# Performance work log

Measured on AMD Instinct MI355X. Metric: run time of the kernel, lower is better.

## Reference

```python
import jax, jax.numpy as jnp
import numpy as np

B, N, C, H, W = 32, 32, 3, 32, 32
HID, OUT = 256, 128


def _conv(x, w, b):
    y = jax.lax.conv_general_dilated(
        x, w, window_strides=(1, 1), padding="SAME",
        dimension_numbers=("NCHW", "OIHW", "NCHW"))
    return y + b[None, :, None, None]


def _sage(h, lw, lb, rw):
    # PyG SAGEConv with mean aggregation on a fully-connected graph (no self-loops):
    # agg_i = (sum_j h_j - h_i) / (N-1); out = agg @ lw.T + lb + h @ rw.T
    n = h.shape[1]
    agg = (jnp.sum(h, axis=1, keepdims=True) - h) / (n - 1)
    return jnp.einsum('bnd,od->bno', agg, lw) + lb + jnp.einsum('bnd,od->bno', h, rw)


def setup_inputs() -> dict:
    key = jax.random.key(0)
    ks = jax.random.split(key, 16)
    def g(k, shape, scale):
        return jax.random.normal(k, shape, dtype=jnp.float32) * scale
    return {
        "x": jax.random.normal(ks[0], (B, N, C, H, W), dtype=jnp.float32),
        "mask": jnp.ones((B, N), dtype=jnp.float32),
        "conv1_w": g(ks[1], (64, C, 3, 3), 0.1),
        "conv1_b": jnp.zeros((64,), jnp.float32),
        "conv2_w": g(ks[2], (128, 64, 3, 3), 0.05),
        "conv2_b": jnp.zeros((128,), jnp.float32),
        "fc_w": g(ks[3], (HID, 128), 0.08),
        "fc_b": jnp.zeros((HID,), jnp.float32),
        "s1_lw": g(ks[4], (HID, HID), 0.06),
        "s1_lb": jnp.zeros((HID,), jnp.float32),
        "s1_rw": g(ks[5], (HID, HID), 0.06),
        "s2_lw": g(ks[6], (OUT, HID), 0.06),
        "s2_lb": jnp.zeros((OUT,), jnp.float32),
        "s2_rw": g(ks[7], (OUT, HID), 0.06),
    }


def reference(x, mask, conv1_w, conv1_b, conv2_w, conv2_b, fc_w, fc_b,
              s1_lw, s1_lb, s1_rw, s2_lw, s2_lb, s2_rw):
    b, n, c, h, w = x.shape
    z = x.reshape(b * n, c, h, w)
    z = jax.nn.relu(_conv(z, conv1_w, conv1_b))
    z = jax.nn.relu(_conv(z, conv2_w, conv2_b))
    z = jnp.mean(z, axis=(2, 3))                      # AdaptiveAvgPool2d((1,1)) + flatten
    z = z @ fc_w.T + fc_b                             # [B*N, HID]
    z = z.reshape(b, n, -1) * mask[:, :, None]
    z = jax.nn.relu(_sage(z, s1_lw, s1_lb, s1_rw))
    z = _sage(z, s2_lw, s2_lb, s2_rw)                 # [B, N, OUT]
    return z
```

## Files before the change

kernel.cpp:

```cpp
#include <hip/hip_runtime.h>
#include <hip/hip_bf16.h>


typedef __attribute__((ext_vector_type(8))) short bfrag;
typedef __attribute__((ext_vector_type(4))) float f32x4;
typedef __attribute__((ext_vector_type(16))) float f32x16;

static __device__ __forceinline__ unsigned short f2bf(float f) {
    union { float f; unsigned u; } v; v.f = f;
    unsigned r = v.u + 0x7fff + ((v.u >> 16) & 1);
    return (unsigned short)(r >> 16);
}

static __device__ __forceinline__ unsigned cvtpk(float lo, float hi) {
    unsigned r;
    asm("v_cvt_pk_bf16_f32 %0, %1, %2" : "=v"(r) : "v"(lo), "v"(hi));
    return r;
}

static __device__ __forceinline__ void gl_lds16(const short* g, short* l) {
    __builtin_amdgcn_global_load_lds(
        (const __attribute__((address_space(1))) unsigned int*)g,
        (__attribute__((address_space(3))) unsigned int*)l, 16, 0, 0);
}

__global__ __launch_bounds__(256) void prep_kernel(
    const float* __restrict__ s1lw, const float* __restrict__ s1rw,
    const float* __restrict__ s2lw, const float* __restrict__ s2rw,
    const float* __restrict__ c2w, const float* __restrict__ c1w,
    const float* __restrict__ c1b, const float* __restrict__ fcw,
    float* __restrict__ l1T, float* __restrict__ w1pT,
    float* __restrict__ l2T, float* __restrict__ w2pT,
    float* __restrict__ fwT,
    short* __restrict__ w2c, short* __restrict__ w1b) {
    int i = blockIdx.x * 256 + threadIdx.x;
    const float inv31 = 1.f / 31.f;
    if (i < 65536) {
        int o = i >> 8, d = i & 255;
        float lw = s1lw[i];
        float rw = s1rw[i];
        l1T[d * 256 + o]  = lw;
        w1pT[d * 256 + o] = rw - lw * inv31;
    }
    if (i < 32768) {
        int o = i >> 8, d = i & 255;
        float lw = s2lw[i];
        float rw = s2rw[i];
        l2T[d * 128 + o]  = lw;
        w2pT[d * 128 + o] = rw - lw * inv31;
        int o2 = i >> 7, c = i & 127;
        fwT[c * 256 + o2] = fcw[i];
    }
    if (i < 73728) {
        int oc = i / 576, rem = i - oc * 576;
        int ic = rem / 9, tap = rem - ic * 9;
        int widx = tap * 8192 + (ic >> 4) * 2048 + ((ic >> 3) & 1) * 1024
                 + oc * 8 + (ic & 7);
        w2c[widx] = (short)f2bf(c2w[i]);
    }
    if (i < 2048) {
        int oc = i >> 5, k = i & 31;
        float v = (k < 27) ? c1w[oc * 27 + k] : (k == 27 ? c1b[oc] : 0.f);
        w1b[i] = (short)f2bf(v);
    }
}

__global__ __launch_bounds__(256, 2) void fused_conv_kernel(
    const float* __restrict__ x, const short* __restrict__ w1b,
    const short* __restrict__ w2c, const float* __restrict__ b2,
    float* __restrict__ pooled4) {
    const int band = blockIdx.x, img = blockIdx.y;
    __shared__ short xt[3 * 12 * 34];
    __shared__ short c1t[10 * 34 * 72];
    __shared__ short bufB[3][4096];
    __shared__ float wsum[4][128];
    const int t = threadIdx.x;
    const int w = t >> 6, lane = t & 63;
    const int ln15 = lane & 15, q8 = (lane >> 4) * 8;
    const int ln31 = lane & 31, hi = lane >> 5;

    const float* xi = x + img * 3072;
    for (int idx = t; idx < 1224; idx += 256) {
        int c = idx / 408, rem = idx % 408, r = rem / 34, col = rem % 34;
        int y = band * 8 - 2 + r, xx = col - 1;
        float v = 0.f;
        if ((unsigned)y < 32u && (unsigned)xx < 32u) v = xi[c * 1024 + y * 32 + xx];
        xt[idx] = (short)f2bf(v);
    }
    {
        f32x4 z = {0.f, 0.f, 0.f, 0.f};
        for (int i = t; i < 180; i += 256) {
            int r = i / 18, rem = i % 18, side = rem / 9, q = rem % 9;
            *(f32x4*)(c1t + (r * 34 + side * 33) * 72 + q * 8) = z;
        }
    }
    bfrag b1f[4];
#pragma unroll
    for (int ot = 0; ot < 4; ++ot)
        b1f[ot] = *(const bfrag*)(w1b + (ot * 16 + ln15) * 32 + q8);

    int xOff[8]; int kMask[8]; int kOvr[8];
#pragma unroll
    for (int j = 0; j < 8; ++j) {
        int k = q8 + j;
        int c = (k * 57) >> 9;
        int rem = k - 9 * c;
        int dy = (rem * 11) >> 5;
        int dx = rem - 3 * dy;
        int cc = c < 3 ? c : 2;
        xOff[j] = cc * 408 + dy * 34 + dx;
        kMask[j] = (c < 3) ? 0xFFFF : 0;
        kOvr[j]  = (c < 3) ? 0 : (k == 27 ? 0x3F80 : 0);
    }
    __syncthreads();

    {
        const short* src = w2c + t * 8;
        short* dst = (short*)bufB + t * 8;
        gl_lds16(src, dst);
        gl_lds16(src + 2048, dst + 2048);
        gl_lds16(src + 4096, dst + 4096);
        gl_lds16(src + 6144, dst + 6144);
    }

#pragma unroll 1
    for (int pt = 0; pt < 5; ++pt) {
        const int tile = w * 5 + pt;
        const int r = tile >> 1, xcb = (tile & 1) << 4;
        const int baseA = r * 34 + xcb + ln15;
        bfrag a1f;
#pragma unroll
        for (int j = 0; j < 8; ++j)
            a1f[j] = (short)((xt[xOff[j] + baseA] & kMask[j]) | kOvr[j]);
        f32x4 acc1[4];
#pragma unroll
        for (int ot = 0; ot < 4; ++ot) {
#pragma unroll
            for (int rg = 0; rg < 4; ++rg) acc1[ot][rg] = 0.f;
            acc1[ot] = __builtin_amdgcn_mfma_f32_16x16x32_bf16(
                b1f[ot], a1f, acc1[ot], 0, 0, 0);
        }
        const int y = band * 8 - 1 + r;
        const bool valid = (unsigned)y < 32u;
        const int waddr = (r * 34 + xcb + ln15 + 1) * 72 + (lane >> 4) * 4;
#pragma unroll
        for (int ot = 0; ot < 4; ++ot) {
            uint2 pk = {0u, 0u};
            if (valid) {
                pk.x = cvtpk(fmaxf(acc1[ot][0], 0.f), fmaxf(acc1[ot][1], 0.f));
                pk.y = cvtpk(fmaxf(acc1[ot][2], 0.f), fmaxf(acc1[ot][3], 0.f));
            }
            *(uint2*)&c1t[waddr + ot * 16] = pk;
        }
    }
    __syncthreads();

    float b2v[4];
#pragma unroll
    for (int ot = 0; ot < 4; ++ot) b2v[ot] = b2[ot * 32 + ln31];

    f32x16 acc[2][4];
#pragma unroll
    for (int pt = 0; pt < 2; ++pt)
#pragma unroll
        for (int ot = 0; ot < 4; ++ot)
#pragma unroll
            for (int rg = 0; rg < 16; ++rg) acc[pt][ot][rg] = 0.f;

    const int aB0 = (w * 2 * 34 + ln31) * 72 + hi * 8;
    const int aB1 = aB0 + 34 * 72;
    const int bOff = hi * 1024 + ln31 * 8;
    const short* stSrc = w2c + t * 8;
    short* stDst = (short*)bufB + t * 8;

    auto stage = [&](int st) {
        const short* src = stSrc + st * 4096;
        short* dst = stDst + (st % 3) * 4096;
        gl_lds16(src, dst);
        gl_lds16(src + 2048, dst + 2048);
    };
    auto prefB = [&](bfrag* bf, int st) {
        const short* bc = (const short*)bufB + (st % 3) * 4096 + bOff;
#pragma unroll
        for (int kk = 0; kk < 2; ++kk)
#pragma unroll
            for (int ot = 0; ot < 4; ++ot)
                bf[kk * 4 + ot] = *(const bfrag*)(bc + kk * 2048 + ot * 256);
    };
    auto body = [&](int st, const bfrag* bCur, bfrag* bNext) {
        if (st + 2 < 18) stage(st + 2);
        const int tap = st >> 1, kh = st & 1;
        const int dy = (tap * 11) >> 5, dx = tap - 3 * dy;
        const int aOff = (dy * 34 + dx) * 72 + kh * 32;
        bfrag af0 = *(const bfrag*)&c1t[aB0 + aOff];
        bfrag af1 = *(const bfrag*)&c1t[aB0 + aOff + 16];
        bfrag af2 = *(const bfrag*)&c1t[aB1 + aOff];
        bfrag af3 = *(const bfrag*)&c1t[aB1 + aOff + 16];
        if (st + 1 < 18) prefB(bNext, st + 1);
        __builtin_amdgcn_s_setprio(1);
#pragma unroll
        for (int ot = 0; ot < 4; ++ot)
            acc[0][ot] = __builtin_amdgcn_mfma_f32_32x32x16_bf16(
                af0, bCur[ot], acc[0][ot], 0, 0, 0);
#pragma unroll
        for (int ot = 0; ot < 4; ++ot)
            acc[0][ot] = __builtin_amdgcn_mfma_f32_32x32x16_bf16(
                af1, bCur[4 + ot], acc[0][ot], 0, 0, 0);
#pragma unroll
        for (int ot = 0; ot < 4; ++ot)
            acc[1][ot] = __builtin_amdgcn_mfma_f32_32x32x16_bf16(
                af2, bCur[ot], acc[1][ot], 0, 0, 0);
#pragma unroll
        for (int ot = 0; ot < 4; ++ot)
            acc[1][ot] = __builtin_amdgcn_mfma_f32_32x32x16_bf16(
                af3, bCur[4 + ot], acc[1][ot], 0, 0, 0);
        __builtin_amdgcn_s_setprio(0);
        asm volatile("s_waitcnt vmcnt(0)" ::: "memory");
        __builtin_amdgcn_s_barrier();
    };

    bfrag bX[8], bY[8];
    prefB(bX, 0);
#pragma unroll 1
    for (int st = 0; st < 18; st += 2) {
        body(st, bX, bY);
        body(st + 1, bY, bX);
    }

#pragma unroll
    for (int ot = 0; ot < 4; ++ot) {
        float s = 0.f;
#pragma unroll
        for (int pt = 0; pt < 2; ++pt)
#pragma unroll
            for (int rg = 0; rg < 16; ++rg)
                s += fmaxf(acc[pt][ot][rg] + b2v[ot], 0.f);
        s += __shfl_xor(s, 32, 64);
        if (lane < 32) wsum[w][ot * 32 + ln31] = s;
    }
    __syncthreads();
    if (t < 128) {
        pooled4[((size_t)img * 4 + band) * 128 + t] =
            wsum[0][t] + wsum[1][t] + wsum[2][t] + wsum[3][t];
    }
}

__global__ __launch_bounds__(256) void fc_kernel(
    const float* __restrict__ pooled4, const float* __restrict__ fwT,
    const float* __restrict__ fb, const float* __restrict__ mask,
    float* __restrict__ z1) {
    const int g = blockIdx.x;
    __shared__ float m[4][128];
    const int t = threadIdx.x;
    if (t < 128) {
#pragma unroll
        for (int i = 0; i < 4; ++i) {
            const float* p = pooled4 + (size_t)(g * 4 + i) * 4 * 128 + t;
            m[i][t] = (p[0] + p[128] + p[256] + p[384]) * (1.f / 1024.f);
        }
    }
    __syncthreads();
    float a0 = fb[t], a1 = a0, a2 = a0, a3 = a0;
#pragma unroll 4
    for (int c = 0; c < 128; ++c) {
        float wv = fwT[c * 256 + t];
        a0 = fmaf(m[0][c], wv, a0);
        a1 = fmaf(m[1][c], wv, a1);
        a2 = fmaf(m[2][c], wv, a2);
        a3 = fmaf(m[3][c], wv, a3);
    }
    z1[(g * 4 + 0) * 256 + t] = a0 * mask[g * 4 + 0];
    z1[(g * 4 + 1) * 256 + t] = a1 * mask[g * 4 + 1];
    z1[(g * 4 + 2) * 256 + t] = a2 * mask[g * 4 + 2];
    z1[(g * 4 + 3) * 256 + t] = a3 * mask[g * 4 + 3];
}

__global__ __launch_bounds__(256) void sage1_kernel(
    const float* __restrict__ z1, const float* __restrict__ l1T,
    const float* __restrict__ lb, const float* __restrict__ w1pT,
    float* __restrict__ z2) {
    const int bx = blockIdx.x;
    const int bb = bx >> 4, chunk = (bx >> 1) & 7, ohalf = bx & 1;
    __shared__ float h[32 * 256];
    __shared__ float sl[256];
    __shared__ float part[2][128];
    __shared__ float pacc[2][4][128];
    const int t = threadIdx.x;
    const int oo = t & 127, dh = t >> 7;
    const int o = ohalf * 128 + oo;
    const float* zb = z1 + bb * 8192;
    for (int idx = t; idx < 8192; idx += 256) h[idx] = zb[idx];
    __syncthreads();
    {
        float s = 0.f;
#pragma unroll
        for (int n = 0; n < 32; ++n) s += h[n * 256 + t];
        sl[t] = s * (1.f / 31.f);
    }
    __syncthreads();
    const int d0b = dh * 128;
    float c = 0.f;
#pragma unroll 4
    for (int d = 0; d < 128; ++d) c = fmaf(sl[d0b + d], l1T[(d0b + d) * 256 + o], c);
    part[dh][oo] = c;
    float acc[4] = {0.f, 0.f, 0.f, 0.f};
    for (int d = 0; d < 128; d += 4) {
        float wv0 = w1pT[(d0b + d + 0) * 256 + o];
        float wv1 = w1pT[(d0b + d + 1) * 256 + o];
        float wv2 = w1pT[(d0b + d + 2) * 256 + o];
        float wv3 = w1pT[(d0b + d + 3) * 256 + o];
#pragma unroll
        for (int i = 0; i < 4; ++i) {
            f32x4 hv = *(const f32x4*)&h[(chunk * 4 + i) * 256 + d0b + d];
            acc[i] = fmaf(hv[0], wv0, acc[i]);
            acc[i] = fmaf(hv[1], wv1, acc[i]);
            acc[i] = fmaf(hv[2], wv2, acc[i]);
            acc[i] = fmaf(hv[3], wv3, acc[i]);
        }
    }
#pragma unroll
    for (int i = 0; i < 4; ++i) pacc[dh][i][oo] = acc[i];
    __syncthreads();
    const float cf = part[0][oo] + part[1][oo] + lb[o];
#pragma unroll
    for (int ii = 0; ii < 2; ++ii) {
        const int i = dh * 2 + ii;
        float v = cf + pacc[0][i][oo] + pacc[1][i][oo];
        z2[(bb * 32 + chunk * 4 + i) * 256 + o] = fmaxf(v, 0.f);
    }
}

__global__ __launch_bounds__(256) void sage2_kernel(
    const float* __restrict__ z2, const float* __restrict__ l2T,
    const float* __restrict__ lb, const float* __restrict__ w2pT,
    float* __restrict__ out) {
    const int bx = blockIdx.x;
    const int bb = bx >> 4, chunk = bx & 15;
    __shared__ float h[32 * 256];
    __shared__ float sl[256];
    __shared__ float part[2][128];
    __shared__ float pacc[2][2][128];
    const int t = threadIdx.x;
    const int oo = t & 127, dh = t >> 7;
    const float* zb = z2 + bb * 8192;
    for (int idx = t; idx < 8192; idx += 256) h[idx] = zb[idx];
    __syncthreads();
    {
        float s = 0.f;
#pragma unroll
        for (int n = 0; n < 32; ++n) s += h[n * 256 + t];
        sl[t] = s * (1.f / 31.f);
    }
    __syncthreads();
    const int d0b = dh * 128;
    const int n0 = chunk * 2;
    float c = 0.f;
#pragma unroll 4
    for (int d = 0; d < 128; ++d) c = fmaf(sl[d0b + d], l2T[(d0b + d) * 128 + oo], c);
    part[dh][oo] = c;
    float acc[2] = {0.f, 0.f};
    for (int d = 0; d < 128; d += 4) {
        float wv0 = w2pT[(d0b + d + 0) * 128 + oo];
        float wv1 = w2pT[(d0b + d + 1) * 128 + oo];
        float wv2 = w2pT[(d0b + d + 2) * 128 + oo];
        float wv3 = w2pT[(d0b + d + 3) * 128 + oo];
#pragma unroll
        for (int i = 0; i < 2; ++i) {
            f32x4 hv = *(const f32x4*)&h[(n0 + i) * 256 + d0b + d];
            acc[i] = fmaf(hv[0], wv0, acc[i]);
            acc[i] = fmaf(hv[1], wv1, acc[i]);
            acc[i] = fmaf(hv[2], wv2, acc[i]);
            acc[i] = fmaf(hv[3], wv3, acc[i]);
        }
    }
#pragma unroll
    for (int i = 0; i < 2; ++i) pacc[dh][i][oo] = acc[i];
    __syncthreads();
    const float cf = part[0][oo] + part[1][oo] + lb[oo];
    {
        const int i = dh;
        float v = cf + pacc[0][i][oo] + pacc[1][i][oo];
        out[(size_t)(bb * 32 + n0 + i) * 128 + oo] = v;
    }
}

extern "C" void kernel_launch(void* const* d_in, const int* in_sizes, int n_in,
                              void* d_out, int out_size, void* d_ws, size_t ws_size,
                              hipStream_t stream) {
    const float* x    = (const float*)d_in[0];
    const float* mask = (const float*)d_in[1];
    const float* c1w  = (const float*)d_in[2];
    const float* c1b  = (const float*)d_in[3];
    const float* c2w  = (const float*)d_in[4];
    const float* c2b  = (const float*)d_in[5];
    const float* fcw  = (const float*)d_in[6];
    const float* fcb  = (const float*)d_in[7];
    const float* s1lw = (const float*)d_in[8];
    const float* s1lb = (const float*)d_in[9];
    const float* s1rw = (const float*)d_in[10];
    const float* s2lw = (const float*)d_in[11];
    const float* s2lb = (const float*)d_in[12];
    const float* s2rw = (const float*)d_in[13];
    float* out = (float*)d_out;

    char* ws = (char*)d_ws;
    float* pooled4 = (float*)(ws);
    float* z1      = (float*)(ws + 2048u * 1024);
    float* z2      = (float*)(ws + 3072u * 1024);
    float* l1T     = (float*)(ws + 4096u * 1024);
    float* w1pT    = (float*)(ws + 4352u * 1024);
    float* l2T     = (float*)(ws + 4608u * 1024);
    float* w2pT    = (float*)(ws + 4736u * 1024);
    float* fwT     = (float*)(ws + 4864u * 1024);
    short* w2c     = (short*)(ws + 4992u * 1024);
    short* w1b     = (short*)(ws + 5136u * 1024);

    prep_kernel<<<dim3(288), 256, 0, stream>>>(s1lw, s1rw, s2lw, s2rw, c2w, c1w, c1b,
                                               fcw, l1T, w1pT, l2T, w2pT, fwT, w2c, w1b);
    fused_conv_kernel<<<dim3(4, 1024), 256, 0, stream>>>(x, w1b, w2c, c2b, pooled4);
    fc_kernel<<<dim3(256), 256, 0, stream>>>(pooled4, fwT, fcb, mask, z1);
    sage1_kernel<<<dim3(512), 256, 0, stream>>>(z1, l1T, s1lb, w1pT, z2);
    sage2_kernel<<<dim3(512), 256, 0, stream>>>(z2, l2T, s2lb, w2pT, out);
}
```

Measured before the change: 260.7 us.

## Fuse fc, sage1 and sage2 into one per-batch kernel with LDS intermediates

Replaces the three tail kernels (fc, sage1, sage2) with a single 1024-thread kernel per batch that keeps the fc output and the layer-1 output in shared memory. This removes two kernel launches and the global round-trips of the z1/z2 intermediates. In exchange only 32 blocks run on a GPU with many more CUs, so the tail work loses parallelism. Each block also reads the full weight matrices itself.

```diff
diff --git a/kernel.cpp b/kernel.cpp
--- a/kernel.cpp
+++ b/kernel.cpp
@@ -245,142 +245,156 @@
     }
 }
 
-__global__ __launch_bounds__(256) void fc_kernel(
+__global__ __launch_bounds__(1024) void sage_fused_kernel(
     const float* __restrict__ pooled4, const float* __restrict__ fwT,
     const float* __restrict__ fb, const float* __restrict__ mask,
-    float* __restrict__ z1) {
-    const int g = blockIdx.x;
-    __shared__ float m[4][128];
+    const float* __restrict__ l1T, const float* __restrict__ lb1,
+    const float* __restrict__ w1pT,
+    const float* __restrict__ l2T, const float* __restrict__ lb2,
+    const float* __restrict__ w2pT, float* __restrict__ out) {
+    const int bb = blockIdx.x;
+    __shared__ float m[32 * 128];
+    __shared__ float h[32 * 256];
+    __shared__ float z2l[32 * 256];
+    __shared__ float sl[256];
+    __shared__ float cf[256];
+    __shared__ float sc4[4][256];
+    __shared__ float sc8[8][128];
     const int t = threadIdx.x;
+
+    for (int idx = t; idx < 4096; idx += 1024) {
+        int i = idx >> 7, c = idx & 127;
+        const float* p = pooled4 + ((size_t)(bb * 32 + i) * 4) * 128 + c;
+        m[idx] = (p[0] + p[128] + p[256] + p[384]) * (1.f / 1024.f);
+    }
+    __syncthreads();
+
+    {
+        const int o = t & 255, ig = t >> 8;
+        float acc[8];
+#pragma unroll
+        for (int i = 0; i < 8; ++i) acc[i] = 0.f;
+        for (int c0 = 0; c0 < 128; c0 += 4) {
+            float wv0 = fwT[(c0 + 0) * 256 + o];
+            float wv1 = fwT[(c0 + 1) * 256 + o];
+            float wv2 = fwT[(c0 + 2) * 256 + o];
+            float wv3 = fwT[(c0 + 3) * 256 + o];
+#pragma unroll
+            for (int i = 0; i < 8; ++i) {
+                f32x4 hv = *(const f32x4*)&m[(ig * 8 + i) * 128 + c0];
+                acc[i] = fmaf(hv[0], wv0, acc[i]);
+                acc[i] = fmaf(hv[1], wv1, acc[i]);
+                acc[i] = fmaf(hv[2], wv2, acc[i]);
+                acc[i] = fmaf(hv[3], wv3, acc[i]);
+            }
+        }
+        const float b = fb[o];
+#pragma unroll
+        for (int i = 0; i < 8; ++i) {
+            const int n = ig * 8 + i;
+            h[n * 256 + o] = (acc[i] + b) * mask[bb * 32 + n];
+        }
+    }
+    __syncthreads();
+
+    {
+        const int col = t & 255, q = t >> 8;
+        float s = 0.f;
+#pragma unroll
+        for (int n = 0; n < 8; ++n) s += h[(q * 8 + n) * 256 + col];
+        sc4[q][col] = s;
+    }
+    __syncthreads();
+    if (t < 256) sl[t] = (sc4[0][t] + sc4[1][t] + sc4[2][t] + sc4[3][t]) * (1.f / 31.f);
+    __syncthreads();
+
+    {
+        const int o = t & 255, dq = t >> 8;
+        float c = 0.f;
+#pragma unroll 4
+        for (int d = 0; d < 64; ++d)
+            c = fmaf(sl[dq * 64 + d], l1T[(dq * 64 + d) * 256 + o], c);
+        sc4[dq][o] = c;
+    }
+    __syncthreads();
+    if (t < 256) cf[t] = sc4[0][t] + sc4[1][t] + sc4[2][t] + sc4[3][t] + lb1[t];
+    __syncthreads();
+
+    {
+        const int o = t & 255, ng = t >> 8;
+        float acc[8];
+#pragma unroll
+        for (int i = 0; i < 8; ++i) acc[i] = 0.f;
+        for (int d0 = 0; d0 < 256; d0 += 4) {
+            float wv0 = w1pT[(d0 + 0) * 256 + o];
+            float wv1 = w1pT[(d0 + 1) * 256 + o];
+            float wv2 = w1pT[(d0 + 2) * 256 + o];
+            float wv3 = w1pT[(d0 + 3) * 256 + o];
+#pragma unroll
+            for (int i = 0; i < 8; ++i) {
+                f32x4 hv = *(const f32x4*)&h[(ng * 8 + i) * 256 + d0];
+                acc[i] = fmaf(hv[0], wv0, acc[i]);
+                acc[i] = fmaf(hv[1], wv1, acc[i]);
+                acc[i] = fmaf(hv[2], wv2, acc[i]);
+                acc[i] = fmaf(hv[3], wv3, acc[i]);
+            }
+        }
+        const float c1 = cf[o];
+#pragma unroll
+        for (int i = 0; i < 8; ++i)
+            z2l[(ng * 8 + i) * 256 + o] = fmaxf(acc[i] + c1, 0.f);
+    }
+    __syncthreads();
+
+    {
+        const int col = t & 255, q = t >> 8;
+        float s = 0.f;
+#pragma unroll
+        for (int n = 0; n < 8; ++n) s += z2l[(q * 8 + n) * 256 + col];
+        sc4[q][col] = s;
+    }
+    __syncthreads();
+    if (t < 256) sl[t] = (sc4[0][t] + sc4[1][t] + sc4[2][t] + sc4[3][t]) * (1.f / 31.f);
+    __syncthreads();
+
+    {
+        const int o = t & 127, dg = t >> 7;
+        float c = 0.f;
+#pragma unroll 4
+        for (int d = 0; d < 32; ++d)
+            c = fmaf(sl[dg * 32 + d], l2T[(dg * 32 + d) * 128 + o], c);
+        sc8[dg][o] = c;
+    }
+    __syncthreads();
     if (t < 128) {
-#pragma unroll
-        for (int i = 0; i < 4; ++i) {
-            const float* p = pooled4 + (size_t)(g * 4 + i) * 4 * 128 + t;
-            m[i][t] = (p[0] + p[128] + p[256] + p[384]) * (1.f / 1024.f);
-        }
-    }
-    __syncthreads();
-    float a0 = fb[t], a1 = a0, a2 = a0, a3 = a0;
-#pragma unroll 4
-    for (int c = 0; c < 128; ++c) {
-        float wv = fwT[c * 256 + t];
-        a0 = fmaf(m[0][c], wv, a0);
-        a1 = fmaf(m[1][c], wv, a1);
-        a2 = fmaf(m[2][c], wv, a2);
-        a3 = fmaf(m[3][c], wv, a3);
-    }
-    z1[(g * 4 + 0) * 256 + t] = a0 * mask[g * 4 + 0];
-    z1[(g * 4 + 1) * 256 + t] = a1 * mask[g * 4 + 1];
-    z1[(g * 4 + 2) * 256 + t] = a2 * mask[g * 4 + 2];
-    z1[(g * 4 + 3) * 256 + t] = a3 * mask[g * 4 + 3];
-}
-
-__global__ __launch_bounds__(256) void sage1_kernel(
-    const float* __restrict__ z1, const float* __restrict__ l1T,
-    const float* __restrict__ lb, const float* __restrict__ w1pT,
-    float* __restrict__ z2) {
-    const int bx = blockIdx.x;
-    const int bb = bx >> 4, chunk = (bx >> 1) & 7, ohalf = bx & 1;
-    __shared__ float h[32 * 256];
-    __shared__ float sl[256];
-    __shared__ float part[2][128];
-    __shared__ float pacc[2][4][128];
-    const int t = threadIdx.x;
-    const int oo = t & 127, dh = t >> 7;
-    const int o = ohalf * 128 + oo;
-    const float* zb = z1 + bb * 8192;
-    for (int idx = t; idx < 8192; idx += 256) h[idx] = zb[idx];
-    __syncthreads();
-    {
-        float s = 0.f;
-#pragma unroll
-        for (int n = 0; n < 32; ++n) s += h[n * 256 + t];
-        sl[t] = s * (1.f / 31.f);
-    }
-    __syncthreads();
-    const int d0b = dh * 128;
-    float c = 0.f;
-#pragma unroll 4
-    for (int d = 0; d < 128; ++d) c = fmaf(sl[d0b + d], l1T[(d0b + d) * 256 + o], c);
-    part[dh][oo] = c;
-    float acc[4] = {0.f, 0.f, 0.f, 0.f};
-    for (int d = 0; d < 128; d += 4) {
-        float wv0 = w1pT[(d0b + d + 0) * 256 + o];
-        float wv1 = w1pT[(d0b + d + 1) * 256 + o];
-        float wv2 = w1pT[(d0b + d + 2) * 256 + o];
-        float wv3 = w1pT[(d0b + d + 3) * 256 + o];
-#pragma unroll
-        for (int i = 0; i < 4; ++i) {
-            f32x4 hv = *(const f32x4*)&h[(chunk * 4 + i) * 256 + d0b + d];
-            acc[i] = fmaf(hv[0], wv0, acc[i]);
-            acc[i] = fmaf(hv[1], wv1, acc[i]);
-            acc[i] = fmaf(hv[2], wv2, acc[i]);
-            acc[i] = fmaf(hv[3], wv3, acc[i]);
-        }
-    }
-#pragma unroll
-    for (int i = 0; i < 4; ++i) pacc[dh][i][oo] = acc[i];
-    __syncthreads();
-    const float cf = part[0][oo] + part[1][oo] + lb[o];
-#pragma unroll
-    for (int ii = 0; ii < 2; ++ii) {
-        const int i = dh * 2 + ii;
-        float v = cf + pacc[0][i][oo] + pacc[1][i][oo];
-        z2[(bb * 32 + chunk * 4 + i) * 256 + o] = fmaxf(v, 0.f);
-    }
-}
-
-__global__ __launch_bounds__(256) void sage2_kernel(
-    const float* __restrict__ z2, const float* __restrict__ l2T,
-    const float* __restrict__ lb, const float* __restrict__ w2pT,
-    float* __restrict__ out) {
-    const int bx = blockIdx.x;
-    const int bb = bx >> 4, chunk = bx & 15;
-    __shared__ float h[32 * 256];
-    __shared__ float sl[256];
-    __shared__ float part[2][128];
-    __shared__ float pacc[2][2][128];
-    const int t = threadIdx.x;
-    const int oo = t & 127, dh = t >> 7;
-    const float* zb = z2 + bb * 8192;
-    for (int idx = t; idx < 8192; idx += 256) h[idx] = zb[idx];
-    __syncthreads();
-    {
-        float s = 0.f;
-#pragma unroll
-        for (int n = 0; n < 32; ++n) s += h[n * 256 + t];
-        sl[t] = s * (1.f / 31.f);
-    }
-    __syncthreads();
-    const int d0b = dh * 128;
-    const int n0 = chunk * 2;
-    float c = 0.f;
-#pragma unroll 4
-    for (int d = 0; d < 128; ++d) c = fmaf(sl[d0b + d], l2T[(d0b + d) * 128 + oo], c);
-    part[dh][oo] = c;
-    float acc[2] = {0.f, 0.f};
-    for (int d = 0; d < 128; d += 4) {
-        float wv0 = w2pT[(d0b + d + 0) * 128 + oo];
-        float wv1 = w2pT[(d0b + d + 1) * 128 + oo];
-        float wv2 = w2pT[(d0b + d + 2) * 128 + oo];
-        float wv3 = w2pT[(d0b + d + 3) * 128 + oo];
-#pragma unroll
-        for (int i = 0; i < 2; ++i) {
-            f32x4 hv = *(const f32x4*)&h[(n0 + i) * 256 + d0b + d];
-            acc[i] = fmaf(hv[0], wv0, acc[i]);
-            acc[i] = fmaf(hv[1], wv1, acc[i]);
-            acc[i] = fmaf(hv[2], wv2, acc[i]);
-            acc[i] = fmaf(hv[3], wv3, acc[i]);
-        }
-    }
-#pragma unroll
-    for (int i = 0; i < 2; ++i) pacc[dh][i][oo] = acc[i];
-    __syncthreads();
-    const float cf = part[0][oo] + part[1][oo] + lb[oo];
-    {
-        const int i = dh;
-        float v = cf + pacc[0][i][oo] + pacc[1][i][oo];
-        out[(size_t)(bb * 32 + n0 + i) * 128 + oo] = v;
+        cf[t] = sc8[0][t] + sc8[1][t] + sc8[2][t] + sc8[3][t] +
+                sc8[4][t] + sc8[5][t] + sc8[6][t] + sc8[7][t] + lb2[t];
+    }
+    __syncthreads();
+
+    {
+        const int o = t & 127, ng = t >> 7;
+        float acc[4];
+#pragma unroll
+        for (int i = 0; i < 4; ++i) acc[i] = 0.f;
+        for (int d0 = 0; d0 < 256; d0 += 4) {
+            float wv0 = w2pT[(d0 + 0) * 128 + o];
+            float wv1 = w2pT[(d0 + 1) * 128 + o];
+            float wv2 = w2pT[(d0 + 2) * 128 + o];
+            float wv3 = w2pT[(d0 + 3) * 128 + o];
+#pragma unroll
+            for (int i = 0; i < 4; ++i) {
+                f32x4 hv = *(const f32x4*)&z2l[(ng * 4 + i) * 256 + d0];
+                acc[i] = fmaf(hv[0], wv0, acc[i]);
+                acc[i] = fmaf(hv[1], wv1, acc[i]);
+                acc[i] = fmaf(hv[2], wv2, acc[i]);
+                acc[i] = fmaf(hv[3], wv3, acc[i]);
+            }
+        }
+        const float c2 = cf[o];
+#pragma unroll
+        for (int i = 0; i < 4; ++i)
+            out[(size_t)(bb * 32 + ng * 4 + i) * 128 + o] = acc[i] + c2;
     }
 }
 
@@ -405,8 +419,6 @@
 
     char* ws = (char*)d_ws;
     float* pooled4 = (float*)(ws);
-    float* z1      = (float*)(ws + 2048u * 1024);
-    float* z2      = (float*)(ws + 3072u * 1024);
     float* l1T     = (float*)(ws + 4096u * 1024);
     float* w1pT    = (float*)(ws + 4352u * 1024);
     float* l2T     = (float*)(ws + 4608u * 1024);
@@ -418,7 +430,7 @@
     prep_kernel<<<dim3(288), 256, 0, stream>>>(s1lw, s1rw, s2lw, s2rw, c2w, c1w, c1b,
                                                fcw, l1T, w1pT, l2T, w2pT, fwT, w2c, w1b);
     fused_conv_kernel<<<dim3(4, 1024), 256, 0, stream>>>(x, w1b, w2c, c2b, pooled4);
-    fc_kernel<<<dim3(256), 256, 0, stream>>>(pooled4, fwT, fcb, mask, z1);
-    sage1_kernel<<<dim3(512), 256, 0, stream>>>(z1, l1T, s1lb, w1pT, z2);
-    sage2_kernel<<<dim3(512), 256, 0, stream>>>(z2, l2T, s2lb, w2pT, out);
-}
+    sage_fused_kernel<<<dim3(32), 1024, 0, stream>>>(pooled4, fwT, fcb, mask,
+                                                     l1T, s1lb, w1pT,
+                                                     l2T, s2lb, w2pT, out);
+}
```

New measurement: 282.1 us. 1.08x slower.
